# Kernel optimization log

Hardware: AMD Instinct MI355X
Metric: run time of the kernel (lower is better)

Reference implementation:

```python
import jax, jax.numpy as jnp
import numpy as np
import math

D_MODEL = 1024
N_HEADS = 16
HEAD_DIM = D_MODEL // N_HEADS
SEQ_LEN = 8192
INCLUDE_LOCAL = 2


def get_dilated_positions(seq_len, include_local=2):
    # Faithful numpy port of the torch pattern generator (runs once at setup).
    max_attend = include_local + int(math.ceil(math.log2(seq_len + 1)))
    positions = np.zeros((seq_len, max_attend), dtype=np.int64)
    mask = np.zeros((seq_len, max_attend), dtype=bool)
    for i in range(seq_len):
        ap = [i]
        for j in range(1, include_local + 1):
            if i - j >= 0:
                ap.append(i - j)
        k = 2
        while i - 2 ** k >= 0:
            ap.append(i - 2 ** k)
            k += 1
        positions[i, :len(ap)] = ap
        mask[i, :len(ap)] = True
    return positions, mask


def setup_inputs() -> dict:
    key = jax.random.key(0)
    kx, kq, kk, kv, ko = jax.random.split(key, 5)
    x = jax.random.normal(kx, (1, SEQ_LEN, D_MODEL), dtype=jnp.float32)
    # nn.Linear(bias=False) weights, torch layout [out_features, in_features]
    s = 0.02
    q_w = jax.random.normal(kq, (D_MODEL, D_MODEL), dtype=jnp.float32) * s
    k_w = jax.random.normal(kk, (D_MODEL, D_MODEL), dtype=jnp.float32) * s
    v_w = jax.random.normal(kv, (D_MODEL, D_MODEL), dtype=jnp.float32) * s
    o_w = jax.random.normal(ko, (D_MODEL, D_MODEL), dtype=jnp.float32) * s
    pos_np, mask_np = get_dilated_positions(SEQ_LEN, INCLUDE_LOCAL)
    return {
        "x": x,
        "q_w": q_w, "k_w": k_w, "v_w": v_w, "o_w": o_w,
        "positions": jnp.asarray(pos_np),   # (S, A) int64 indices
        "attend_mask": jnp.asarray(mask_np) # (S, A) bool
    }


def reference(x, q_w, k_w, v_w, o_w, positions, attend_mask):
    B, S, _ = x.shape
    H, Dh = N_HEADS, HEAD_DIM
    scale = Dh ** -0.5

    q = (x @ q_w.T).reshape(B, S, H, Dh).transpose(0, 2, 1, 3)  # (B,H,S,Dh)
    k = (x @ k_w.T).reshape(B, S, H, Dh).transpose(0, 2, 1, 3)
    v = (x @ v_w.T).reshape(B, S, H, Dh).transpose(0, 2, 1, 3)

    # Gather K/V at the dilated positions: (B,H,S,A,Dh)
    k_sparse = k[:, :, positions, :]
    v_sparse = v[:, :, positions, :]

    scores = jnp.einsum('bhsd,bhsad->bhsa', q, k_sparse) * scale
    scores = jnp.where(attend_mask[None, None, :, :], scores, -jnp.inf)
    attn = jax.nn.softmax(scores, axis=-1)  # dropout p in eval / 0.0 -> identity

    out = jnp.einsum('bhsa,bhsad->bhsd', attn, v_sparse)
    out = out.transpose(0, 2, 1, 3).reshape(B, S, D_MODEL)
    return out @ o_w.T
```

## Files before the change

kernel.cpp:

```cpp
#include <hip/hip_runtime.h>
#include <hip/hip_bf16.h>

typedef __bf16 bf16_t;
typedef __bf16 bf16x4 __attribute__((ext_vector_type(4)));
typedef __bf16 bf16x8 __attribute__((ext_vector_type(8)));
typedef float floatx4 __attribute__((ext_vector_type(4)));

#define SEQ    8192
#define DM     1024
#define NHEADS 16
#define HDIM   64

__device__ __forceinline__ void async_ld16(bf16_t* lds, const bf16_t* g) {
  __builtin_amdgcn_global_load_lds(
      (__attribute__((address_space(1))) void*)g,
      (__attribute__((address_space(3))) void*)lds, 16, 0, 0);
}

__global__ __launch_bounds__(256)
void cvt_all(const float* __restrict__ x,  const float* __restrict__ qw,
             const float* __restrict__ kw, const float* __restrict__ vw,
             const float* __restrict__ ow,
             bf16_t* __restrict__ Xb,  bf16_t* __restrict__ QWb,
             bf16_t* __restrict__ KWb, bf16_t* __restrict__ VWb,
             bf16_t* __restrict__ OWb) {
  const int b = blockIdx.x;
  const float* in; bf16_t* out; int g;
  if (b < 8192) { in = x; out = Xb; g = b; }
  else {
    const int w  = (b - 8192) >> 10;
    const int wb = (b - 8192) & 1023;
    switch (w) {
      case 0:  in = qw; out = QWb; break;
      case 1:  in = kw; out = KWb; break;
      case 2:  in = vw; out = VWb; break;
      default: in = ow; out = OWb; break;
    }
    g = wb;
  }
  const int idx = (g * 256 + threadIdx.x) * 4;
  float4 v = *(const float4*)(in + idx);
  bf16x4 o = { (bf16_t)v.x, (bf16_t)v.y, (bf16_t)v.z, (bf16_t)v.w };
  *(bf16x4*)(out + idx) = o;
}

__global__ __launch_bounds__(256)
void gemm_qkv_fused(const bf16_t* __restrict__ A,
                    const bf16_t* __restrict__ Bq, const bf16_t* __restrict__ Bk,
                    const bf16_t* __restrict__ Bv,
                    bf16_t* __restrict__ Cq, bf16_t* __restrict__ Ck,
                    bf16_t* __restrict__ Cv)
{
  constexpr int Kdim = DM;
  __shared__ __attribute__((aligned(16))) bf16_t sA[128 * 32];
  __shared__ __attribute__((aligned(16))) bf16_t sB[3][64 * 32];

  const int tid  = threadIdx.x;
  const int wave = tid >> 6;
  const int lane = tid & 63;
  const int quad = lane >> 4;
  const int r16  = lane & 15;
  const int wr   = (wave >> 1) * 64;
  const int wc   = (wave & 1) * 32;

  const size_t arow = (size_t)blockIdx.x * 128 + wave * 32 + (lane >> 2);
  const bf16_t* Ag = A + arow * Kdim + (lane & 3) * 8;
  const size_t brow = (size_t)blockIdx.y * 64 + wave * 16 + (lane >> 2);
  const bf16_t* Bqg = Bq + brow * Kdim + (lane & 3) * 8;
  const bf16_t* Bkg = Bk + brow * Kdim + (lane & 3) * 8;
  const bf16_t* Bvg = Bv + brow * Kdim + (lane & 3) * 8;
  bf16_t* sAw  = sA    + wave * 32 * 32;
  bf16_t* sB0w = sB[0] + wave * 16 * 32;
  bf16_t* sB1w = sB[1] + wave * 16 * 32;
  bf16_t* sB2w = sB[2] + wave * 16 * 32;

  floatx4 acc[3][4][2];
  #pragma unroll
  for (int t = 0; t < 3; ++t)
    #pragma unroll
    for (int i = 0; i < 4; ++i)
      #pragma unroll
      for (int j = 0; j < 2; ++j)
        acc[t][i][j] = (floatx4)(0.0f);

  for (int ko = 0; ko < Kdim; ko += 32) {
    async_ld16(sAw,           Ag + ko);
    async_ld16(sAw + 16 * 32, Ag + 16 * Kdim + ko);
    async_ld16(sB0w, Bqg + ko);
    async_ld16(sB1w, Bkg + ko);
    async_ld16(sB2w, Bvg + ko);
    __syncthreads();

    bf16x8 af[4];
    #pragma unroll
    for (int mi = 0; mi < 4; ++mi)
      af[mi] = *(const bf16x8*)&sA[(wr + mi * 16 + r16) * 32 + quad * 8];
    bf16x8 bfr[3][2];
    #pragma unroll
    for (int t = 0; t < 3; ++t)
      #pragma unroll
      for (int ni = 0; ni < 2; ++ni)
        bfr[t][ni] = *(const bf16x8*)&sB[t][(wc + ni * 16 + r16) * 32 + quad * 8];

    #pragma unroll
    for (int t = 0; t < 3; ++t)
      #pragma unroll
      for (int mi = 0; mi < 4; ++mi)
        #pragma unroll
        for (int ni = 0; ni < 2; ++ni)
          acc[t][mi][ni] = __builtin_amdgcn_mfma_f32_16x16x32_bf16(af[mi], bfr[t][ni], acc[t][mi][ni], 0, 0, 0);

    __syncthreads();
  }

  const int crow0 = blockIdx.x * 128 + wr + quad * 4;
  const int ccol0 = blockIdx.y * 64 + wc + r16;
  #pragma unroll
  for (int t = 0; t < 3; ++t) {
    bf16_t* C = (t == 0) ? Cq : (t == 1) ? Ck : Cv;
    #pragma unroll
    for (int mi = 0; mi < 4; ++mi)
      #pragma unroll
      for (int ni = 0; ni < 2; ++ni)
        #pragma unroll
        for (int r = 0; r < 4; ++r)
          C[(size_t)(crow0 + mi * 16 + r) * DM + (ccol0 + ni * 16)] = (bf16_t)acc[t][mi][ni][r];
  }
}

__global__ __launch_bounds__(256)
void gemm_out(const bf16_t* __restrict__ A, const bf16_t* __restrict__ B,
              float* __restrict__ C)
{
  constexpr int Kdim = DM;
  __shared__ __attribute__((aligned(16))) bf16_t sA[128 * 32];
  __shared__ __attribute__((aligned(16))) bf16_t sB[128 * 32];

  const int tid  = threadIdx.x;
  const int wave = tid >> 6;
  const int lane = tid & 63;
  const int quad = lane >> 4;
  const int r16  = lane & 15;
  const int wr   = (wave >> 1) * 64;
  const int wc   = (wave & 1) * 64;

  const size_t arow0 = (size_t)blockIdx.x * 128 + wave * 32 + (lane >> 2);
  const size_t brow0 = (size_t)blockIdx.y * 128 + wave * 32 + (lane >> 2);
  const bf16_t* Ag = A + arow0 * Kdim + (lane & 3) * 8;
  const bf16_t* Bg = B + brow0 * Kdim + (lane & 3) * 8;
  bf16_t* sAw = sA + wave * 32 * 32;
  bf16_t* sBw = sB + wave * 32 * 32;

  floatx4 acc[4][4];
  #pragma unroll
  for (int i = 0; i < 4; ++i)
    #pragma unroll
    for (int j = 0; j < 4; ++j)
      acc[i][j] = (floatx4)(0.0f);

  for (int ko = 0; ko < Kdim; ko += 32) {
    async_ld16(sAw,           Ag + ko);
    async_ld16(sAw + 16 * 32, Ag + 16 * Kdim + ko);
    async_ld16(sBw,           Bg + ko);
    async_ld16(sBw + 16 * 32, Bg + 16 * Kdim + ko);
    __syncthreads();

    bf16x8 af[4], bfr[4];
    #pragma unroll
    for (int mi = 0; mi < 4; ++mi)
      af[mi] = *(const bf16x8*)&sA[(wr + mi * 16 + r16) * 32 + quad * 8];
    #pragma unroll
    for (int ni = 0; ni < 4; ++ni)
      bfr[ni] = *(const bf16x8*)&sB[(wc + ni * 16 + r16) * 32 + quad * 8];

    #pragma unroll
    for (int mi = 0; mi < 4; ++mi)
      #pragma unroll
      for (int ni = 0; ni < 4; ++ni)
        acc[mi][ni] = __builtin_amdgcn_mfma_f32_16x16x32_bf16(af[mi], bfr[ni], acc[mi][ni], 0, 0, 0);

    __syncthreads();
  }

  const int crow0 = blockIdx.x * 128 + wr + quad * 4;
  const int ccol0 = blockIdx.y * 128 + wc + r16;
  #pragma unroll
  for (int mi = 0; mi < 4; ++mi)
    #pragma unroll
    for (int ni = 0; ni < 4; ++ni)
      #pragma unroll
      for (int r = 0; r < 4; ++r)
        C[(size_t)(crow0 + mi * 16 + r) * DM + (ccol0 + ni * 16)] = acc[mi][ni][r];
}

__global__ __launch_bounds__(256)
void dilated_attn(const bf16_t* __restrict__ Q, const bf16_t* __restrict__ K,
                  const bf16_t* __restrict__ V, bf16_t* O)
{
  const int lane = threadIdx.x & 63;
  const int i = blockIdx.x * 4 + (threadIdx.x >> 6);
  const size_t base = (size_t)i * DM + lane * 16;

  bf16x8 q0 = *(const bf16x8*)(Q + base);
  bf16x8 q1 = *(const bf16x8*)(Q + base + 8);
  float qf[16];
  #pragma unroll
  for (int j = 0; j < 8; ++j) { qf[j] = (float)q0[j] * 0.125f; qf[j + 8] = (float)q1[j] * 0.125f; }

  float m = -INFINITY, l = 0.0f;
  float acc[16];
  #pragma unroll
  for (int j = 0; j < 16; ++j) acc[j] = 0.0f;

  int off = 1;
  size_t rb = base;
  bf16x8 k0 = *(const bf16x8*)(K + rb), k1 = *(const bf16x8*)(K + rb + 8);
  bf16x8 v0 = *(const bf16x8*)(V + rb), v1 = *(const bf16x8*)(V + rb + 8);

  while (true) {
    const int pn = i - off;
    const bool more = (pn >= 0);
    bf16x8 nk0, nk1, nv0, nv1;
    if (more) {
      size_t nb = (size_t)pn * DM + lane * 16;
      nk0 = *(const bf16x8*)(K + nb); nk1 = *(const bf16x8*)(K + nb + 8);
      nv0 = *(const bf16x8*)(V + nb); nv1 = *(const bf16x8*)(V + nb + 8);
    }

    float sc = 0.0f;
    #pragma unroll
    for (int j = 0; j < 8; ++j) sc += qf[j] * (float)k0[j] + qf[j + 8] * (float)k1[j];
    sc += __shfl_xor(sc, 1, 64);
    sc += __shfl_xor(sc, 2, 64);

    float mn = fmaxf(m, sc);
    float co = __expf(m - mn);
    float w  = __expf(sc - mn);
    l = l * co + w;
    m = mn;
    #pragma unroll
    for (int j = 0; j < 8; ++j) {
      acc[j]     = acc[j]     * co + w * (float)v0[j];
      acc[j + 8] = acc[j + 8] * co + w * (float)v1[j];
    }

    if (!more) break;
    k0 = nk0; k1 = nk1; v0 = nv0; v1 = nv1;
    off <<= 1;
  }

  const float inv = 1.0f / l;
  bf16x8 o0, o1;
  #pragma unroll
  for (int j = 0; j < 8; ++j) { o0[j] = (bf16_t)(acc[j] * inv); o1[j] = (bf16_t)(acc[j + 8] * inv); }
  *(bf16x8*)(O + base)     = o0;
  *(bf16x8*)(O + base + 8) = o1;
}

extern "C" void kernel_launch(void* const* d_in, const int* in_sizes, int n_in,
                              void* d_out, int out_size, void* d_ws, size_t ws_size,
                              hipStream_t stream) {
  (void)in_sizes; (void)n_in; (void)out_size; (void)ws_size;
  const float* x  = (const float*)d_in[0];
  const float* qw = (const float*)d_in[1];
  const float* kw = (const float*)d_in[2];
  const float* vw = (const float*)d_in[3];
  const float* ow = (const float*)d_in[4];
  float* out = (float*)d_out;

  bf16_t* Xb  = (bf16_t*)d_ws;
  bf16_t* Qb  = Xb  + (size_t)SEQ * DM;
  bf16_t* Kb  = Qb  + (size_t)SEQ * DM;
  bf16_t* Vb  = Kb  + (size_t)SEQ * DM;
  bf16_t* QWb = Vb  + (size_t)SEQ * DM;
  bf16_t* KWb = QWb + (size_t)DM * DM;
  bf16_t* VWb = KWb + (size_t)DM * DM;
  bf16_t* OWb = VWb + (size_t)DM * DM;
  bf16_t* AO  = Qb;

  cvt_all<<<dim3(8192 + 4096), dim3(256), 0, stream>>>(x, qw, kw, vw, ow,
                                                       Xb, QWb, KWb, VWb, OWb);

  dim3 block(256);
  gemm_qkv_fused<<<dim3(SEQ / 128, DM / 64), block, 0, stream>>>(Xb, QWb, KWb, VWb, Qb, Kb, Vb);
  dilated_attn<<<dim3(SEQ / 4), block, 0, stream>>>(Qb, Kb, Vb, AO);
  gemm_out<<<dim3(SEQ / 128, DM / 128), block, 0, stream>>>(AO, OWb, out);
}
```

Baseline: 231.7 us.

## Retile QKV and output GEMMs, unroll dilated attention loop, swizzle block order

Result: slower. 247.7 us (+6.9%).

```diff
diff --git a/kernel.cpp b/kernel.cpp
--- a/kernel.cpp
+++ b/kernel.cpp
@@ -45,15 +45,81 @@
 }
 
 __global__ __launch_bounds__(256)
-void gemm_qkv_fused(const bf16_t* __restrict__ A,
-                    const bf16_t* __restrict__ Bq, const bf16_t* __restrict__ Bk,
-                    const bf16_t* __restrict__ Bv,
-                    bf16_t* __restrict__ Cq, bf16_t* __restrict__ Ck,
-                    bf16_t* __restrict__ Cv)
+void gemm_qkv(const bf16_t* __restrict__ A,
+              const bf16_t* __restrict__ Bq, const bf16_t* __restrict__ Bk,
+              const bf16_t* __restrict__ Bv,
+              bf16_t* __restrict__ Cq, bf16_t* __restrict__ Ck, bf16_t* __restrict__ Cv)
+{
+  const bf16_t* B = (blockIdx.z == 0) ? Bq : (blockIdx.z == 1) ? Bk : Bv;
+  bf16_t*       C = (blockIdx.z == 0) ? Cq : (blockIdx.z == 1) ? Ck : Cv;
+  constexpr int Kdim = DM;
+  __shared__ __attribute__((aligned(16))) bf16_t sA[128 * 32];
+  __shared__ __attribute__((aligned(16))) bf16_t sB[128 * 32];
+
+  const int tid  = threadIdx.x;
+  const int wave = tid >> 6;
+  const int lane = tid & 63;
+  const int quad = lane >> 4;
+  const int r16  = lane & 15;
+  const int wr   = (wave >> 1) * 64;
+  const int wc   = (wave & 1) * 64;
+
+  const size_t arow0 = (size_t)blockIdx.x * 128 + wave * 32 + (lane >> 2);
+  const size_t brow0 = (size_t)blockIdx.y * 128 + wave * 32 + (lane >> 2);
+  const bf16_t* Ag = A + arow0 * Kdim + (lane & 3) * 8;
+  const bf16_t* Bg = B + brow0 * Kdim + (lane & 3) * 8;
+  bf16_t* sAw = sA + wave * 32 * 32;
+  bf16_t* sBw = sB + wave * 32 * 32;
+
+  floatx4 acc[4][4];
+  #pragma unroll
+  for (int i = 0; i < 4; ++i)
+    #pragma unroll
+    for (int j = 0; j < 4; ++j)
+      acc[i][j] = (floatx4)(0.0f);
+
+  for (int ko = 0; ko < Kdim; ko += 32) {
+    async_ld16(sAw,           Ag + ko);
+    async_ld16(sAw + 16 * 32, Ag + 16 * Kdim + ko);
+    async_ld16(sBw,           Bg + ko);
+    async_ld16(sBw + 16 * 32, Bg + 16 * Kdim + ko);
+    __syncthreads();
+
+    bf16x8 af[4], bfr[4];
+    #pragma unroll
+    for (int mi = 0; mi < 4; ++mi)
+      af[mi] = *(const bf16x8*)&sA[(wr + mi * 16 + r16) * 32 + quad * 8];
+    #pragma unroll
+    for (int ni = 0; ni < 4; ++ni)
+      bfr[ni] = *(const bf16x8*)&sB[(wc + ni * 16 + r16) * 32 + quad * 8];
+
+    #pragma unroll
+    for (int mi = 0; mi < 4; ++mi)
+      #pragma unroll
+      for (int ni = 0; ni < 4; ++ni)
+        acc[mi][ni] = __builtin_amdgcn_mfma_f32_16x16x32_bf16(af[mi], bfr[ni], acc[mi][ni], 0, 0, 0);
+
+    __syncthreads();
+  }
+
+  const int crow0 = blockIdx.x * 128 + wr + quad * 4;
+  const int ccol0 = blockIdx.y * 128 + wc + r16;
+  #pragma unroll
+  for (int mi = 0; mi < 4; ++mi)
+    #pragma unroll
+    for (int ni = 0; ni < 4; ++ni)
+      #pragma unroll
+      for (int r = 0; r < 4; ++r)
+        C[(size_t)(crow0 + mi * 16 + r) * DM + (ccol0 + ni * 16)] = (bf16_t)acc[mi][ni][r];
+}
+
+__global__ __launch_bounds__(256)
+void gemm_out(const bf16_t* __restrict__ A, const bf16_t* __restrict__ B,
+              float* __restrict__ C)
 {
   constexpr int Kdim = DM;
   __shared__ __attribute__((aligned(16))) bf16_t sA[128 * 32];
-  __shared__ __attribute__((aligned(16))) bf16_t sB[3][64 * 32];
+  __shared__ __attribute__((aligned(16))) bf16_t sB[64 * 32];
 
   const int tid  = threadIdx.x;
   const int wave = tid >> 6;
@@ -64,130 +130,48 @@
   const int wc   = (wave & 1) * 32;
 
   const size_t arow = (size_t)blockIdx.x * 128 + wave * 32 + (lane >> 2);
+  const size_t brow = (size_t)blockIdx.y * 64 + wave * 16 + (lane >> 2);
   const bf16_t* Ag = A + arow * Kdim + (lane & 3) * 8;
-  const size_t brow = (size_t)blockIdx.y * 64 + wave * 16 + (lane >> 2);
-  const bf16_t* Bqg = Bq + brow * Kdim + (lane & 3) * 8;
-  const bf16_t* Bkg = Bk + brow * Kdim + (lane & 3) * 8;
-  const bf16_t* Bvg = Bv + brow * Kdim + (lane & 3) * 8;
-  bf16_t* sAw  = sA    + wave * 32 * 32;
-  bf16_t* sB0w = sB[0] + wave * 16 * 32;
-  bf16_t* sB1w = sB[1] + wave * 16 * 32;
-  bf16_t* sB2w = sB[2] + wave * 16 * 32;
-
-  floatx4 acc[3][4][2];
-  #pragma unroll
-  for (int t = 0; t < 3; ++t)
-    #pragma unroll
-    for (int i = 0; i < 4; ++i)
-      #pragma unroll
-      for (int j = 0; j < 2; ++j)
-        acc[t][i][j] = (floatx4)(0.0f);
-
-  for (int ko = 0; ko < Kdim; ko += 32) {
-    async_ld16(sAw,           Ag + ko);
-    async_ld16(sAw + 16 * 32, Ag + 16 * Kdim + ko);
-    async_ld16(sB0w, Bqg + ko);
-    async_ld16(sB1w, Bkg + ko);
-    async_ld16(sB2w, Bvg + ko);
-    __syncthreads();
-
-    bf16x8 af[4];
-    #pragma unroll
-    for (int mi = 0; mi < 4; ++mi)
-      af[mi] = *(const bf16x8*)&sA[(wr + mi * 16 + r16) * 32 + quad * 8];
-    bf16x8 bfr[3][2];
-    #pragma unroll
-    for (int t = 0; t < 3; ++t)
-      #pragma unroll
-      for (int ni = 0; ni < 2; ++ni)
-        bfr[t][ni] = *(const bf16x8*)&sB[t][(wc + ni * 16 + r16) * 32 + quad * 8];
-
-    #pragma unroll
-    for (int t = 0; t < 3; ++t)
-      #pragma unroll
-      for (int mi = 0; mi < 4; ++mi)
-        #pragma unroll
-        for (int ni = 0; ni < 2; ++ni)
-          acc[t][mi][ni] = __builtin_amdgcn_mfma_f32_16x16x32_bf16(af[mi], bfr[t][ni], acc[t][mi][ni], 0, 0, 0);
-
-    __syncthreads();
-  }
-
-  const int crow0 = blockIdx.x * 128 + wr + quad * 4;
-  const int ccol0 = blockIdx.y * 64 + wc + r16;
-  #pragma unroll
-  for (int t = 0; t < 3; ++t) {
-    bf16_t* C = (t == 0) ? Cq : (t == 1) ? Ck : Cv;
-    #pragma unroll
-    for (int mi = 0; mi < 4; ++mi)
-      #pragma unroll
-      for (int ni = 0; ni < 2; ++ni)
-        #pragma unroll
-        for (int r = 0; r < 4; ++r)
-          C[(size_t)(crow0 + mi * 16 + r) * DM + (ccol0 + ni * 16)] = (bf16_t)acc[t][mi][ni][r];
-  }
-}
-
-__global__ __launch_bounds__(256)
-void gemm_out(const bf16_t* __restrict__ A, const bf16_t* __restrict__ B,
-              float* __restrict__ C)
-{
-  constexpr int Kdim = DM;
-  __shared__ __attribute__((aligned(16))) bf16_t sA[128 * 32];
-  __shared__ __attribute__((aligned(16))) bf16_t sB[128 * 32];
-
-  const int tid  = threadIdx.x;
-  const int wave = tid >> 6;
-  const int lane = tid & 63;
-  const int quad = lane >> 4;
-  const int r16  = lane & 15;
-  const int wr   = (wave >> 1) * 64;
-  const int wc   = (wave & 1) * 64;
-
-  const size_t arow0 = (size_t)blockIdx.x * 128 + wave * 32 + (lane >> 2);
-  const size_t brow0 = (size_t)blockIdx.y * 128 + wave * 32 + (lane >> 2);
-  const bf16_t* Ag = A + arow0 * Kdim + (lane & 3) * 8;
-  const bf16_t* Bg = B + brow0 * Kdim + (lane & 3) * 8;
+  const bf16_t* Bg = B + brow * Kdim + (lane & 3) * 8;
   bf16_t* sAw = sA + wave * 32 * 32;
-  bf16_t* sBw = sB + wave * 32 * 32;
-
-  floatx4 acc[4][4];
+  bf16_t* sBw = sB + wave * 16 * 32;
+
+  floatx4 acc[4][2];
   #pragma unroll
   for (int i = 0; i < 4; ++i)
     #pragma unroll
-    for (int j = 0; j < 4; ++j)
+    for (int j = 0; j < 2; ++j)
       acc[i][j] = (floatx4)(0.0f);
 
   for (int ko = 0; ko < Kdim; ko += 32) {
     async_ld16(sAw,           Ag + ko);
     async_ld16(sAw + 16 * 32, Ag + 16 * Kdim + ko);
     async_ld16(sBw,           Bg + ko);
-    async_ld16(sBw + 16 * 32, Bg + 16 * Kdim + ko);
-    __syncthreads();
-
-    bf16x8 af[4], bfr[4];
+    __syncthreads();
+
+    bf16x8 af[4], bfr[2];
     #pragma unroll
     for (int mi = 0; mi < 4; ++mi)
       af[mi] = *(const bf16x8*)&sA[(wr + mi * 16 + r16) * 32 + quad * 8];
     #pragma unroll
-    for (int ni = 0; ni < 4; ++ni)
+    for (int ni = 0; ni < 2; ++ni)
       bfr[ni] = *(const bf16x8*)&sB[(wc + ni * 16 + r16) * 32 + quad * 8];
 
     #pragma unroll
     for (int mi = 0; mi < 4; ++mi)
       #pragma unroll
-      for (int ni = 0; ni < 4; ++ni)
+      for (int ni = 0; ni < 2; ++ni)
         acc[mi][ni] = __builtin_amdgcn_mfma_f32_16x16x32_bf16(af[mi], bfr[ni], acc[mi][ni], 0, 0, 0);
 
     __syncthreads();
   }
 
   const int crow0 = blockIdx.x * 128 + wr + quad * 4;
-  const int ccol0 = blockIdx.y * 128 + wc + r16;
+  const int ccol0 = blockIdx.y * 64 + wc + r16;
   #pragma unroll
   for (int mi = 0; mi < 4; ++mi)
     #pragma unroll
-    for (int ni = 0; ni < 4; ++ni)
+    for (int ni = 0; ni < 2; ++ni)
       #pragma unroll
       for (int r = 0; r < 4; ++r)
         C[(size_t)(crow0 + mi * 16 + r) * DM + (ccol0 + ni * 16)] = acc[mi][ni][r];
@@ -198,7 +182,8 @@
                   const bf16_t* __restrict__ V, bf16_t* O)
 {
   const int lane = threadIdx.x & 63;
-  const int i = blockIdx.x * 4 + (threadIdx.x >> 6);
+  const int qb   = (blockIdx.x & 7) * 256 + (blockIdx.x >> 3);
+  const int i    = qb * 4 + (threadIdx.x >> 6);
   const size_t base = (size_t)i * DM + lane * 16;
 
   bf16x8 q0 = *(const bf16x8*)(Q + base);
@@ -212,26 +197,21 @@
   #pragma unroll
   for (int j = 0; j < 16; ++j) acc[j] = 0.0f;
 
-  int off = 1;
-  size_t rb = base;
-  bf16x8 k0 = *(const bf16x8*)(K + rb), k1 = *(const bf16x8*)(K + rb + 8);
-  bf16x8 v0 = *(const bf16x8*)(V + rb), v1 = *(const bf16x8*)(V + rb + 8);
-
-  while (true) {
-    const int pn = i - off;
-    const bool more = (pn >= 0);
-    bf16x8 nk0, nk1, nv0, nv1;
-    if (more) {
-      size_t nb = (size_t)pn * DM + lane * 16;
-      nk0 = *(const bf16x8*)(K + nb); nk1 = *(const bf16x8*)(K + nb + 8);
-      nv0 = *(const bf16x8*)(V + nb); nv1 = *(const bf16x8*)(V + nb + 8);
-    }
+  #pragma unroll
+  for (int t = 0; t < 14; ++t) {
+    const int offv  = (t == 0) ? 0 : (1 << (t - 1));
+    const int pn    = i - offv;
+    const bool valid = (pn >= 0);
+    const size_t nb = (size_t)(valid ? pn : 0) * DM + lane * 16;
+    bf16x8 k0 = *(const bf16x8*)(K + nb), k1 = *(const bf16x8*)(K + nb + 8);
+    bf16x8 v0 = *(const bf16x8*)(V + nb), v1 = *(const bf16x8*)(V + nb + 8);
 
     float sc = 0.0f;
     #pragma unroll
     for (int j = 0; j < 8; ++j) sc += qf[j] * (float)k0[j] + qf[j + 8] * (float)k1[j];
     sc += __shfl_xor(sc, 1, 64);
     sc += __shfl_xor(sc, 2, 64);
+    sc = valid ? sc : -INFINITY;
 
     float mn = fmaxf(m, sc);
     float co = __expf(m - mn);
@@ -243,10 +223,6 @@
       acc[j]     = acc[j]     * co + w * (float)v0[j];
       acc[j + 8] = acc[j + 8] * co + w * (float)v1[j];
     }
-
-    if (!more) break;
-    k0 = nk0; k1 = nk1; v0 = nv0; v1 = nv1;
-    off <<= 1;
   }
 
   const float inv = 1.0f / l;
@@ -282,7 +258,7 @@
                                                        Xb, QWb, KWb, VWb, OWb);
 
   dim3 block(256);
-  gemm_qkv_fused<<<dim3(SEQ / 128, DM / 64), block, 0, stream>>>(Xb, QWb, KWb, VWb, Qb, Kb, Vb);
+  gemm_qkv<<<dim3(SEQ / 128, DM / 128, 3), block, 0, stream>>>(Xb, QWb, KWb, VWb, Qb, Kb, Vb);
   dilated_attn<<<dim3(SEQ / 4), block, 0, stream>>>(Qb, Kb, Vb, AO);
-  gemm_out<<<dim3(SEQ / 128, DM / 128), block, 0, stream>>>(AO, OWb, out);
-}
+  gemm_out<<<dim3(SEQ / 128, DM / 64), block, 0, stream>>>(AO, OWb, out);
+}
```
